# Optimization experiments

Hardware: AMD Instinct MI355X
Metric: run time of the kernel (lower is better)

Reference implementation:

```python
import jax, jax.numpy as jnp
import numpy as np

D_MODEL = 768
NUM_HEADS = 12
D_K = D_MODEL // NUM_HEADS
D_FF = 2048
LN_EPS = 1e-3  # Keras LayerNormalization default
B, S = 4, 2048


def layer_norm(x, gamma, beta):
    mu = jnp.mean(x, axis=-1, keepdims=True)
    var = jnp.var(x, axis=-1, keepdims=True)
    return (x - mu) * jax.lax.rsqrt(var + LN_EPS) * gamma + beta


def setup_inputs() -> dict:
    key = jax.random.key(0)
    ks = jax.random.split(key, 16)
    sd = 0.02
    inp = {
        "x": jax.random.normal(ks[0], (B, S, D_MODEL), dtype=jnp.float32),
        "src_mask": jnp.zeros((B, 1, 1, S), dtype=jnp.float32),
        "Wq": jax.random.normal(ks[1], (D_MODEL, D_MODEL), jnp.float32) * sd,
        "bq": jnp.zeros((D_MODEL,), jnp.float32),
        "Wk": jax.random.normal(ks[2], (D_MODEL, D_MODEL), jnp.float32) * sd,
        "bk": jnp.zeros((D_MODEL,), jnp.float32),
        "Wv": jax.random.normal(ks[3], (D_MODEL, D_MODEL), jnp.float32) * sd,
        "bv": jnp.zeros((D_MODEL,), jnp.float32),
        "Wo": jax.random.normal(ks[4], (D_MODEL, D_MODEL), jnp.float32) * sd,
        "bo": jnp.zeros((D_MODEL,), jnp.float32),
        "W1": jax.random.normal(ks[5], (D_MODEL, D_FF), jnp.float32) * sd,
        "b1": jnp.zeros((D_FF,), jnp.float32),
        "W2": jax.random.normal(ks[6], (D_FF, D_MODEL), jnp.float32) * sd,
        "b2": jnp.zeros((D_MODEL,), jnp.float32),
        "gamma1": jnp.ones((D_MODEL,), jnp.float32),
        "beta1": jnp.zeros((D_MODEL,), jnp.float32),
        "gamma2": jnp.ones((D_MODEL,), jnp.float32),
        "beta2": jnp.zeros((D_MODEL,), jnp.float32),
    }
    return inp


def encoder_layer(x, src_mask, Wq, bq, Wk, bk, Wv, bv, Wo, bo, W1, b1, W2, b2,
                  gamma1, beta1, gamma2, beta2):
    b, s, _ = x.shape
    def heads(t):  # [B,S,D] -> [B,H,S,Dk]
        return t.reshape(b, s, NUM_HEADS, D_K).transpose(0, 2, 1, 3)
    Q = heads(x @ Wq + bq)
    K = heads(x @ Wk + bk)
    V = heads(x @ Wv + bv)
    scores = jnp.einsum("bhqd,bhkd->bhqk", Q, K) / jnp.sqrt(jnp.float32(D_K))
    scores = scores + src_mask * (-1e9)
    probs = jax.nn.softmax(scores, axis=-1)
    attn = jnp.einsum("bhqk,bhkd->bhqd", probs, V)
    attn = attn.transpose(0, 2, 1, 3).reshape(b, s, D_MODEL)
    attn_out = attn @ Wo + bo
    # dropout is identity at inference
    x1 = layer_norm(x + attn_out, gamma1, beta1)
    ff = jax.nn.relu(x1 @ W1 + b1) @ W2 + b2
    return layer_norm(x1 + ff, gamma2, beta2)


def reference(x, src_mask, Wq, bq, Wk, bk, Wv, bv, Wo, bo, W1, b1, W2, b2,
              gamma1, beta1, gamma2, beta2):
    return encoder_layer(x, src_mask, Wq, bq, Wk, bk, Wv, bv, Wo, bo,
                         W1, b1, W2, b2, gamma1, beta1, gamma2, beta2)
```

## Files before the change

kernel.cpp:

```cpp
#include <hip/hip_runtime.h>


typedef unsigned short u16;
typedef __bf16 bf16x8 __attribute__((ext_vector_type(8)));
typedef __bf16 bf16x4 __attribute__((ext_vector_type(4)));
typedef unsigned short u16x8 __attribute__((ext_vector_type(8)));
typedef float f32x4 __attribute__((ext_vector_type(4)));

#define D_MODEL 768
#define D_FF    2048
#define NH      12
#define DK      64
#define S_LEN   2048
#define M_TOK   8192

#define QSCALE   0.18033688011112042f
#define MSCALE  -1.4426950408889634e9f

__device__ __forceinline__ float bf2f(u16 v) {
    union { unsigned u; float f; } c; c.u = ((unsigned)v) << 16; return c.f;
}
__device__ __forceinline__ void st_bf(u16* p, float v) { *(__bf16*)p = (__bf16)v; }

__device__ __forceinline__ void gload_lds16(const void* g, void* l) {
    __builtin_amdgcn_global_load_lds(
        (const __attribute__((address_space(1))) void*)g,
        (__attribute__((address_space(3))) void*)l, 16, 0, 0);
}

__global__ __launch_bounds__(256)
void prep_k(const float* __restrict__ x, const float* __restrict__ Wq,
            const float* __restrict__ Wk, const float* __restrict__ Wv,
            const float* __restrict__ Wo, const float* __restrict__ W1,
            const float* __restrict__ W2, u16* __restrict__ xb,
            u16* __restrict__ WqkvT, u16* __restrict__ WoT,
            u16* __restrict__ W1T, u16* __restrict__ W2T) {
    __shared__ float t[32][33];
    const int id = blockIdx.x, tid = threadIdx.x;
    if (id >= 5376) {
        const int i = ((id - 5376) * 256 + tid) * 4;
        const float4 v = *(const float4*)(x + i);
        __bf16 o[4] = {(__bf16)v.x, (__bf16)v.y, (__bf16)v.z, (__bf16)v.w};
        *(bf16x4*)(xb + i) = *(bf16x4*)o;
        return;
    }
    const float* in; u16* out; int R, C, bx, by;
    if (id < 2304) {
        const int z = id / 576, r = id % 576;
        in = z == 0 ? Wq : (z == 1 ? Wk : (z == 2 ? Wv : Wo));
        out = z == 3 ? WoT : WqkvT + z * 768 * 768;
        R = 768; C = 768; bx = (r % 24) * 32; by = (r / 24) * 32;
    } else if (id < 3840) {
        const int r = id - 2304;
        in = W1; out = W1T; R = 768; C = 2048;
        bx = (r % 64) * 32; by = (r / 64) * 32;
    } else {
        const int r = id - 3840;
        in = W2; out = W2T; R = 2048; C = 768;
        bx = (r % 24) * 32; by = (r / 24) * 32;
    }
    const int tx = tid & 31, ty = tid >> 5;
#pragma unroll
    for (int i = 0; i < 32; i += 8)
        t[ty + i][tx] = in[(size_t)(by + ty + i) * C + bx + tx];
    __syncthreads();
#pragma unroll
    for (int i = 0; i < 32; i += 8)
        st_bf(&out[(size_t)(bx + ty + i) * R + by + tx], t[tx][ty + i]);
}

__global__ __launch_bounds__(256, 2)
void qkv4p_k(const u16* __restrict__ A, const u16* __restrict__ Bt,
             const float* __restrict__ bq, const float* __restrict__ bk,
             const float* __restrict__ bv, u16* __restrict__ Qb,
             u16* __restrict__ Kb, u16* __restrict__ Vt) {
    __shared__ __align__(16) u16 AB[2][16384];
    const int tid = threadIdx.x, lane = tid & 63;
    const int w = tid >> 6;
    const int wm2 = w >> 1, wn2 = w & 1;
    const int r16 = lane & 15, qd = lane >> 4;
    const int qdx = (qd ^ ((r16 >> 1) & 3)) << 3;
    const int m0 = blockIdx.x * 128, n0 = blockIdx.y * 128;
    const int K = D_MODEL, NT = 12;

    const u16* aS[4]; const u16* bS[4];
#pragma unroll
    for (int l = 0; l < 4; ++l) {
        const int f = l * 256 + tid;
        const int row = (f >> 2) & 127, ks = f >> 9;
        const int e = (((f & 3) ^ ((f >> 3) & 3)) << 3);
        aS[l] = A  + (size_t)(m0 + row) * K + ks * 32 + e;
        bS[l] = Bt + (size_t)(n0 + row) * K + ks * 32 + e;
    }

#pragma unroll
    for (int l = 0; l < 4; ++l) {
        gload_lds16(aS[l], &AB[0][(l * 256 + tid) * 8]);
        gload_lds16(bS[l], &AB[0][8192 + (l * 256 + tid) * 8]);
    }
    asm volatile("s_waitcnt vmcnt(0)" ::: "memory");
    __builtin_amdgcn_s_barrier();

    f32x4 acc[4][4] = {};
    bf16x8 af[4][2], bfr[4][2];
    const int arow0 = wm2 * 64 + r16;
    const int brow0 = wn2 * 64 + r16;

    for (int t = 0; t < NT; ++t) {
        const int cur = t & 1, nxt = cur ^ 1;
        const u16* ab = AB[cur];
        const int ka = (t + 1) * 64;
        const bool more = (t + 1) < NT;

#pragma unroll
        for (int mt = 0; mt < 4; ++mt)
#pragma unroll
            for (int ks = 0; ks < 2; ++ks)
                af[mt][ks] = *(const bf16x8*)&ab[ks * 4096 + (arow0 + mt * 16) * 32 + qdx];
#pragma unroll
        for (int nt = 0; nt < 2; ++nt)
#pragma unroll
            for (int ks = 0; ks < 2; ++ks)
                bfr[nt][ks] = *(const bf16x8*)&ab[8192 + ks * 4096 + (brow0 + nt * 16) * 32 + qdx];
        if (more) {
#pragma unroll
            for (int l = 0; l < 4; ++l)
                gload_lds16(aS[l] + ka, &AB[nxt][(l * 256 + tid) * 8]);
        }
        __builtin_amdgcn_s_setprio(1);
#pragma unroll
        for (int mt = 0; mt < 4; ++mt)
#pragma unroll
            for (int nt = 0; nt < 2; ++nt)
#pragma unroll
                for (int ks = 0; ks < 2; ++ks)
                    acc[mt][nt] = __builtin_amdgcn_mfma_f32_16x16x32_bf16(bfr[nt][ks], af[mt][ks], acc[mt][nt], 0, 0, 0);
        __builtin_amdgcn_s_setprio(0);
        __builtin_amdgcn_s_barrier();

#pragma unroll
        for (int nt = 2; nt < 4; ++nt)
#pragma unroll
            for (int ks = 0; ks < 2; ++ks)
                bfr[nt][ks] = *(const bf16x8*)&ab[8192 + ks * 4096 + (brow0 + nt * 16) * 32 + qdx];
        if (more) {
#pragma unroll
            for (int l = 0; l < 4; ++l)
                gload_lds16(bS[l] + ka, &AB[nxt][8192 + (l * 256 + tid) * 8]);
        }
        __builtin_amdgcn_s_setprio(1);
#pragma unroll
        for (int mt = 0; mt < 4; ++mt)
#pragma unroll
            for (int nt = 2; nt < 4; ++nt)
#pragma unroll
                for (int ks = 0; ks < 2; ++ks)
                    acc[mt][nt] = __builtin_amdgcn_mfma_f32_16x16x32_bf16(bfr[nt][ks], af[mt][ks], acc[mt][nt], 0, 0, 0);
        __builtin_amdgcn_s_setprio(0);

        if (more) {
            asm volatile("s_waitcnt vmcnt(0)" ::: "memory");
            __builtin_amdgcn_s_barrier();
        }
    }

    const int sel = n0 < 768 ? 0 : (n0 < 1536 ? 1 : 2);
    const float* bias = sel == 0 ? bq : (sel == 1 ? bk : bv);
    const float scale = sel == 0 ? QSCALE : 1.0f;
    const int nbase = n0 - sel * 768;

#pragma unroll
    for (int nt = 0; nt < 4; ++nt) {
        const int nb = nbase + wn2 * 64 + nt * 16 + qd * 4;
        const float4 bvv = *(const float4*)&bias[nb];
        const float b4[4] = {bvv.x, bvv.y, bvv.z, bvv.w};
#pragma unroll
        for (int mi = 0; mi < 4; ++mi) {
            const int m = m0 + wm2 * 64 + mi * 16 + r16;
            if (sel < 2) {
                __bf16 pk[4];
#pragma unroll
                for (int rr = 0; rr < 4; ++rr)
                    pk[rr] = (__bf16)((acc[mi][nt][rr] + b4[rr]) * scale);
                u16* dst = (sel == 0 ? Qb : Kb) + (size_t)m * D_MODEL + nb;
                *(bf16x4*)dst = *(bf16x4*)pk;
            } else {
                const int bb = m >> 11, npb = m & 2047;
#pragma unroll
                for (int rr = 0; rr < 4; ++rr) {
                    const int col = nb + rr, h = col >> 6, d = col & 63;
                    st_bf(&Vt[(((size_t)(bb * NH + h)) * DK + d) * S_LEN + npb],
                          acc[mi][nt][rr] + b4[rr]);
                }
            }
        }
    }
}

__global__ __launch_bounds__(256, 2)
void g4p_k(const u16* __restrict__ A, const u16* __restrict__ Bt,
           const float* __restrict__ bias, u16* __restrict__ Cout,
           int N, int K) {
    __shared__ __align__(16) u16 AB[2][16384];
    const int tid = threadIdx.x, lane = tid & 63;
    const int w = tid >> 6;
    const int wm2 = w >> 1, wn2 = w & 1;
    const int r16 = lane & 15, qd = lane >> 4;
    const int qdx = (qd ^ ((r16 >> 1) & 3)) << 3;
    const int m0 = blockIdx.x * 128, n0 = blockIdx.y * 128;
    const int NT = K >> 6;

    const u16* aS[4]; const u16* bS[4];
#pragma unroll
    for (int l = 0; l < 4; ++l) {
        const int f = l * 256 + tid;
        const int row = (f >> 2) & 127, ks = f >> 9;
        const int e = (((f & 3) ^ ((f >> 3) & 3)) << 3);
        aS[l] = A  + (size_t)(m0 + row) * K + ks * 32 + e;
        bS[l] = Bt + (size_t)(n0 + row) * K + ks * 32 + e;
    }

#pragma unroll
    for (int l = 0; l < 4; ++l) {
        gload_lds16(aS[l], &AB[0][(l * 256 + tid) * 8]);
        gload_lds16(bS[l], &AB[0][8192 + (l * 256 + tid) * 8]);
    }
    asm volatile("s_waitcnt vmcnt(0)" ::: "memory");
    __builtin_amdgcn_s_barrier();

    f32x4 acc[4][4] = {};
    bf16x8 af[4][2], bfr[4][2];
    const int arow0 = wm2 * 64 + r16;
    const int brow0 = wn2 * 64 + r16;

    for (int t = 0; t < NT; ++t) {
        const int cur = t & 1, nxt = cur ^ 1;
        const u16* ab = AB[cur];
        const int ka = (t + 1) * 64;
        const bool more = (t + 1) < NT;

#pragma unroll
        for (int mt = 0; mt < 4; ++mt)
#pragma unroll
            for (int ks = 0; ks < 2; ++ks)
                af[mt][ks] = *(const bf16x8*)&ab[ks * 4096 + (arow0 + mt * 16) * 32 + qdx];
#pragma unroll
        for (int nt = 0; nt < 2; ++nt)
#pragma unroll
            for (int ks = 0; ks < 2; ++ks)
                bfr[nt][ks] = *(const bf16x8*)&ab[8192 + ks * 4096 + (brow0 + nt * 16) * 32 + qdx];
        if (more) {
#pragma unroll
            for (int l = 0; l < 4; ++l)
                gload_lds16(aS[l] + ka, &AB[nxt][(l * 256 + tid) * 8]);
        }
        __builtin_amdgcn_s_setprio(1);
#pragma unroll
        for (int mt = 0; mt < 4; ++mt)
#pragma unroll
            for (int nt = 0; nt < 2; ++nt)
#pragma unroll
                for (int ks = 0; ks < 2; ++ks)
                    acc[mt][nt] = __builtin_amdgcn_mfma_f32_16x16x32_bf16(bfr[nt][ks], af[mt][ks], acc[mt][nt], 0, 0, 0);
        __builtin_amdgcn_s_setprio(0);
        __builtin_amdgcn_s_barrier();

#pragma unroll
        for (int nt = 2; nt < 4; ++nt)
#pragma unroll
            for (int ks = 0; ks < 2; ++ks)
                bfr[nt][ks] = *(const bf16x8*)&ab[8192 + ks * 4096 + (brow0 + nt * 16) * 32 + qdx];
        if (more) {
#pragma unroll
            for (int l = 0; l < 4; ++l)
                gload_lds16(bS[l] + ka, &AB[nxt][8192 + (l * 256 + tid) * 8]);
        }
        __builtin_amdgcn_s_setprio(1);
#pragma unroll
        for (int mt = 0; mt < 4; ++mt)
#pragma unroll
            for (int nt = 2; nt < 4; ++nt)
#pragma unroll
                for (int ks = 0; ks < 2; ++ks)
                    acc[mt][nt] = __builtin_amdgcn_mfma_f32_16x16x32_bf16(bfr[nt][ks], af[mt][ks], acc[mt][nt], 0, 0, 0);
        __builtin_amdgcn_s_setprio(0);

        if (more) {
            asm volatile("s_waitcnt vmcnt(0)" ::: "memory");
            __builtin_amdgcn_s_barrier();
        }
    }

#pragma unroll
    for (int nt = 0; nt < 4; ++nt) {
        const int nb = n0 + wn2 * 64 + nt * 16 + qd * 4;
        const float4 bv = *(const float4*)&bias[nb];
        const float b4[4] = {bv.x, bv.y, bv.z, bv.w};
#pragma unroll
        for (int mi = 0; mi < 4; ++mi) {
            const int m = m0 + wm2 * 64 + mi * 16 + r16;
            __bf16 pk[4];
#pragma unroll
            for (int rr = 0; rr < 4; ++rr)
                pk[rr] = (__bf16)(acc[mi][nt][rr] + b4[rr]);
            *(bf16x4*)&Cout[(size_t)m * N + nb] = *(bf16x4*)pk;
        }
    }
}

__global__ __launch_bounds__(512, 2)
void ff1_k(const u16* __restrict__ A, const u16* __restrict__ Bt,
           const float* __restrict__ bias, u16* __restrict__ C) {
    __shared__ __align__(16) u16 AB[2][32768];
    const int tid = threadIdx.x, lane = tid & 63;
    const int w = tid >> 6;
    const int wm2 = w >> 2, wn4 = w & 3;
    const int r16 = lane & 15, qd = lane >> 4;
    const int qdx = (qd ^ ((r16 >> 1) & 3)) << 3;
    const int m0 = blockIdx.x * 256, n0 = blockIdx.y * 256;
    const int K = D_MODEL, NT = 12;

    const u16* aS[4]; const u16* bS[4];
#pragma unroll
    for (int l = 0; l < 4; ++l) {
        const int f = l * 512 + tid;
        const int row = (f >> 2) & 255, ks = f >> 10;
        const int e = (((f & 3) ^ ((f >> 3) & 3)) << 3);
        aS[l] = A  + (size_t)(m0 + row) * K + ks * 32 + e;
        bS[l] = Bt + (size_t)(n0 + row) * K + ks * 32 + e;
    }

#pragma unroll
    for (int l = 0; l < 4; ++l) {
        gload_lds16(aS[l], &AB[0][(l * 512 + tid) * 8]);
        gload_lds16(bS[l], &AB[0][16384 + (l * 512 + tid) * 8]);
    }
    asm volatile("s_waitcnt vmcnt(0)" ::: "memory");
    __builtin_amdgcn_s_barrier();

    f32x4 acc[8][4] = {};
    bf16x8 af[4][2], bfr[4][2];
    const int arow0 = wm2 * 128 + r16;
    const int brow0 = wn4 * 64 + r16;

    for (int t = 0; t < NT; ++t) {
        const int cur = t & 1, nxt = cur ^ 1;
        const u16* ab = AB[cur];
        const int ka = (t + 1) * 64;
        const bool more = (t + 1) < NT;

#pragma unroll
        for (int mt = 0; mt < 4; ++mt)
#pragma unroll
            for (int ks = 0; ks < 2; ++ks)
                af[mt][ks] = *(const bf16x8*)&ab[ks * 8192 + (arow0 + mt * 16) * 32 + qdx];
#pragma unroll
        for (int nt = 0; nt < 2; ++nt)
#pragma unroll
            for (int ks = 0; ks < 2; ++ks)
                bfr[nt][ks] = *(const bf16x8*)&ab[16384 + ks * 8192 + (brow0 + nt * 16) * 32 + qdx];
        if (more) {
#pragma unroll
            for (int l = 0; l < 4; ++l)
                gload_lds16(aS[l] + ka, &AB[nxt][(l * 512 + tid) * 8]);
        }
        __builtin_amdgcn_s_setprio(1);
#pragma unroll
        for (int mt = 0; mt < 4; ++mt)
#pragma unroll
            for (int nt = 0; nt < 2; ++nt)
#pragma unroll
                for (int ks = 0; ks < 2; ++ks)
                    acc[mt][nt] = __builtin_amdgcn_mfma_f32_16x16x32_bf16(bfr[nt][ks], af[mt][ks], acc[mt][nt], 0, 0, 0);
        __builtin_amdgcn_s_setprio(0);
        __builtin_amdgcn_s_barrier();

#pragma unroll
        for (int nt = 2; nt < 4; ++nt)
#pragma unroll
            for (int ks = 0; ks < 2; ++ks)
                bfr[nt][ks] = *(const bf16x8*)&ab[16384 + ks * 8192 + (brow0 + nt * 16) * 32 + qdx];
        if (more) {
#pragma unroll
            for (int l = 0; l < 4; ++l)
                gload_lds16(bS[l] + ka, &AB[nxt][16384 + (l * 512 + tid) * 8]);
        }
        __builtin_amdgcn_s_setprio(1);
#pragma unroll
        for (int mt = 0; mt < 4; ++mt)
#pragma unroll
            for (int nt = 2; nt < 4; ++nt)
#pragma unroll
                for (int ks = 0; ks < 2; ++ks)
                    acc[mt][nt] = __builtin_amdgcn_mfma_f32_16x16x32_bf16(bfr[nt][ks], af[mt][ks], acc[mt][nt], 0, 0, 0);
        __builtin_amdgcn_s_setprio(0);
        __builtin_amdgcn_s_barrier();

#pragma unroll
        for (int mt = 0; mt < 4; ++mt)
#pragma unroll
            for (int ks = 0; ks < 2; ++ks)
                af[mt][ks] = *(const bf16x8*)&ab[ks * 8192 + (arow0 + 64 + mt * 16) * 32 + qdx];
        __builtin_amdgcn_s_setprio(1);
#pragma unroll
        for (int mt = 0; mt < 4; ++mt)
#pragma unroll
            for (int nt = 0; nt < 2; ++nt)
#pragma unroll
                for (int ks = 0; ks < 2; ++ks)
                    acc[4 + mt][nt] = __builtin_amdgcn_mfma_f32_16x16x32_bf16(bfr[nt][ks], af[mt][ks], acc[4 + mt][nt], 0, 0, 0);
        __builtin_amdgcn_s_setprio(0);
        __builtin_amdgcn_s_barrier();

        __builtin_amdgcn_s_setprio(1);
#pragma unroll
        for (int mt = 0; mt < 4; ++mt)
#pragma unroll
            for (int nt = 2; nt < 4; ++nt)
#pragma unroll
                for (int ks = 0; ks < 2; ++ks)
                    acc[4 + mt][nt] = __builtin_amdgcn_mfma_f32_16x16x32_bf16(bfr[nt][ks], af[mt][ks], acc[4 + mt][nt], 0, 0, 0);
        __builtin_amdgcn_s_setprio(0);

        if (more) {
            asm volatile("s_waitcnt vmcnt(0)" ::: "memory");
            __builtin_amdgcn_s_barrier();
        }
    }

#pragma unroll
    for (int nt = 0; nt < 4; ++nt) {
        const int nb = n0 + wn4 * 64 + nt * 16 + qd * 4;
        const float4 bv = *(const float4*)&bias[nb];
        const float b4[4] = {bv.x, bv.y, bv.z, bv.w};
#pragma unroll
        for (int mi = 0; mi < 8; ++mi) {
            const int m = m0 + wm2 * 128 + (mi >> 2) * 64 + (mi & 3) * 16 + r16;
            __bf16 pk[4];
#pragma unroll
            for (int rr = 0; rr < 4; ++rr)
                pk[rr] = (__bf16)fmaxf(acc[mi][nt][rr] + b4[rr], 0.0f);
            *(bf16x4*)&C[(size_t)m * D_FF + nb] = *(bf16x4*)pk;
        }
    }
}

#define TS 72

__global__ __launch_bounds__(256, 3)
void attn_k(const u16* __restrict__ Qg, const u16* __restrict__ Kg,
            const u16* __restrict__ Vtg, const float* __restrict__ maskg,
            u16* __restrict__ Og) {
    const int tid = threadIdx.x, lane = tid & 63, w = tid >> 6;
    const int qh = w & 1, kh = w >> 1;
    const int r16 = lane & 15, qd = lane >> 4;
    const int q0 = blockIdx.x * 128;
    const int h = blockIdx.y, b = blockIdx.z;

    __shared__ __align__(16) u16 sm[(64 + 64 + 128) * TS];
    u16* Ks  = sm;
    u16* Vts = sm + 64 * TS;
    u16* Ps  = sm + 128 * TS;

    bf16x8 qa[4][2];
#pragma unroll
    for (int mt = 0; mt < 4; ++mt)
#pragma unroll
        for (int ks = 0; ks < 2; ++ks)
            qa[mt][ks] = *(const bf16x8*)(Qg +
                ((size_t)((b * S_LEN + q0 + qh * 64 + mt * 16 + r16) * NH + h)) * DK +
                ks * 32 + qd * 8);

    const int srow = tid >> 3, sc = (tid & 7) << 3;
    const u16* vsrc = Vtg + (((size_t)(b * NH + h)) * DK) * S_LEN;
    u16x8 kreg[2], vreg[2];
#pragma unroll
    for (int it = 0; it < 2; ++it) {
        const int row = srow + it * 32;
        kreg[it] = *(const u16x8*)(Kg + ((size_t)((b * S_LEN + row) * NH + h)) * DK + sc);
        vreg[it] = *(const u16x8*)(vsrc + (size_t)row * S_LEN + sc);
    }

    float l_i[4] = {0.0f, 0.0f, 0.0f, 0.0f};
    f32x4 Oacc[4][4] = {};

    for (int kt = 0; kt < S_LEN / 64; ++kt) {
        const int ks0 = kt * 64;

#pragma unroll
        for (int it = 0; it < 2; ++it) {
            const int row = srow + it * 32;
            *(u16x8*)&Ks[row * TS + sc]  = kreg[it];
            *(u16x8*)&Vts[row * TS + sc] = vreg[it];
        }

        float4 mrow[2];
#pragma unroll
        for (int nt = 0; nt < 2; ++nt) {
            const float4 mm = ((const float4*)(maskg + (size_t)b * S_LEN + ks0))[kh * 8 + nt * 4 + qd];
            mrow[nt].x = mm.x * MSCALE; mrow[nt].y = mm.y * MSCALE;
            mrow[nt].z = mm.z * MSCALE; mrow[nt].w = mm.w * MSCALE;
        }
        __syncthreads();

        f32x4 sa[4][2];
#pragma unroll
        for (int mt = 0; mt < 4; ++mt)
#pragma unroll
            for (int nt = 0; nt < 2; ++nt) {
                sa[mt][nt][0] = mrow[nt].x; sa[mt][nt][1] = mrow[nt].y;
                sa[mt][nt][2] = mrow[nt].z; sa[mt][nt][3] = mrow[nt].w;
            }
#pragma unroll
        for (int ks = 0; ks < 2; ++ks) {
            bf16x8 kb[2];
#pragma unroll
            for (int nt = 0; nt < 2; ++nt)
                kb[nt] = *(const bf16x8*)&Ks[(kh * 32 + nt * 16 + r16) * TS + ks * 32 + qd * 8];
            __builtin_amdgcn_s_setprio(1);
#pragma unroll
            for (int mt = 0; mt < 4; ++mt)
#pragma unroll
                for (int nt = 0; nt < 2; ++nt)
                    sa[mt][nt] = __builtin_amdgcn_mfma_f32_16x16x32_bf16(kb[nt], qa[mt][ks], sa[mt][nt], 0, 0, 0);
            __builtin_amdgcn_s_setprio(0);
        }

#pragma unroll
        for (int mt = 0; mt < 4; ++mt) {
            float rsum = 0.0f;
#pragma unroll
            for (int nt = 0; nt < 2; ++nt) {
                sa[mt][nt][0] = __builtin_amdgcn_exp2f(sa[mt][nt][0]);
                sa[mt][nt][1] = __builtin_amdgcn_exp2f(sa[mt][nt][1]);
                sa[mt][nt][2] = __builtin_amdgcn_exp2f(sa[mt][nt][2]);
                sa[mt][nt][3] = __builtin_amdgcn_exp2f(sa[mt][nt][3]);
                rsum += sa[mt][nt][0] + sa[mt][nt][1] + sa[mt][nt][2] + sa[mt][nt][3];
            }
            rsum += __shfl_xor(rsum, 16);
            rsum += __shfl_xor(rsum, 32);
            l_i[mt] += rsum;
        }

#pragma unroll
        for (int mt = 0; mt < 4; ++mt)
#pragma unroll
            for (int nt = 0; nt < 2; ++nt) {
                __bf16 pk[4];
#pragma unroll
                for (int rr = 0; rr < 4; ++rr) pk[rr] = (__bf16)sa[mt][nt][rr];
                *(bf16x4*)&Ps[(qh * 64 + mt * 16 + r16) * TS + kh * 32 + nt * 16 + qd * 4] = *(bf16x4*)pk;
            }

        if (kt + 1 < S_LEN / 64) {
            const int ns0 = ks0 + 64;
#pragma unroll
            for (int it = 0; it < 2; ++it) {
                const int row = srow + it * 32;
                kreg[it] = *(const u16x8*)(Kg + ((size_t)((b * S_LEN + ns0 + row) * NH + h)) * DK + sc);
                vreg[it] = *(const u16x8*)(vsrc + (size_t)row * S_LEN + ns0 + sc);
            }
        }

        {
            bf16x8 pa[4], vb[4];
#pragma unroll
            for (int mt = 0; mt < 4; ++mt)
                pa[mt] = *(const bf16x8*)&Ps[(qh * 64 + mt * 16 + r16) * TS + kh * 32 + qd * 8];
#pragma unroll
            for (int vt = 0; vt < 4; ++vt)
                vb[vt] = *(const bf16x8*)&Vts[(vt * 16 + r16) * TS + kh * 32 + qd * 8];
            __builtin_amdgcn_s_setprio(1);
#pragma unroll
            for (int mt = 0; mt < 4; ++mt)
#pragma unroll
                for (int vt = 0; vt < 4; ++vt)
                    Oacc[mt][vt] = __builtin_amdgcn_mfma_f32_16x16x32_bf16(pa[mt], vb[vt], Oacc[mt][vt], 0, 0, 0);
            __builtin_amdgcn_s_setprio(0);
        }
        __syncthreads();
    }

    __syncthreads();
    float* mb  = (float*)sm;
    float* lsm = mb + 128 * 64;
    if (kh == 0) {
#pragma unroll
        for (int mt = 0; mt < 4; ++mt) {
            if (qd == 0) lsm[(qh * 4 + mt) * 16 + r16] = l_i[mt];
#pragma unroll
            for (int vt = 0; vt < 4; ++vt)
#pragma unroll
                for (int rr = 0; rr < 4; ++rr)
                    mb[(qh * 64 + mt * 16 + qd * 4 + rr) * 64 + vt * 16 + r16] = Oacc[mt][vt][rr];
        }
    }
    __syncthreads();
    if (kh == 1) {
#pragma unroll
        for (int mt = 0; mt < 4; ++mt) {
            const float linv = 1.0f / (l_i[mt] + lsm[(qh * 4 + mt) * 16 + r16]);
#pragma unroll
            for (int rr = 0; rr < 4; ++rr) {
                const float lr = __shfl(linv, qd * 4 + rr);
                const int qrow = q0 + qh * 64 + mt * 16 + qd * 4 + rr;
#pragma unroll
                for (int vt = 0; vt < 4; ++vt) {
                    const float o = Oacc[mt][vt][rr] +
                        mb[(qh * 64 + mt * 16 + qd * 4 + rr) * 64 + vt * 16 + r16];
                    st_bf(&Og[((size_t)((b * S_LEN + qrow) * NH + h)) * DK + vt * 16 + r16],
                          o * lr);
                }
            }
        }
    }
}

__global__ __launch_bounds__(256, 4)
void resln_k(const u16* __restrict__ xb, const u16* __restrict__ yb,
             const float* __restrict__ gamma, const float* __restrict__ beta,
             u16* __restrict__ outb, float* __restrict__ outf) {
    const int row = blockIdx.x, tid = threadIdx.x;
    const int lane = tid & 63, w = tid >> 6;
    __shared__ float redS[4], redS2[4];
    const size_t base = (size_t)row * D_MODEL;
    float h[3], s = 0.0f, s2 = 0.0f;
#pragma unroll
    for (int i = 0; i < 3; ++i) {
        const int c = i * 256 + tid;
        const float v = bf2f(xb[base + c]) + bf2f(yb[base + c]);
        h[i] = v; s += v; s2 += v * v;
    }
#pragma unroll
    for (int off = 32; off >= 1; off >>= 1) { s += __shfl_xor(s, off); s2 += __shfl_xor(s2, off); }
    if (lane == 0) { redS[w] = s; redS2[w] = s2; }
    __syncthreads();
    s  = redS[0] + redS[1] + redS[2] + redS[3];
    s2 = redS2[0] + redS2[1] + redS2[2] + redS2[3];
    const float mu  = s * (1.0f / D_MODEL);
    const float var = s2 * (1.0f / D_MODEL) - mu * mu;
    const float rstd = rsqrtf(var + 1e-3f);
#pragma unroll
    for (int i = 0; i < 3; ++i) {
        const int c = i * 256 + tid;
        const float o = (h[i] - mu) * rstd * gamma[c] + beta[c];
        if (outb) st_bf(&outb[base + c], o);
        if (outf) outf[base + c] = o;
    }
}

extern "C" void kernel_launch(void* const* d_in, const int* in_sizes, int n_in,
                              void* d_out, int out_size, void* d_ws, size_t ws_size,
                              hipStream_t stream) {
    (void)in_sizes; (void)n_in; (void)out_size; (void)ws_size;
    const float* x    = (const float*)d_in[0];
    const float* mask = (const float*)d_in[1];
    const float* Wq = (const float*)d_in[2];  const float* bq  = (const float*)d_in[3];
    const float* Wk = (const float*)d_in[4];  const float* bk  = (const float*)d_in[5];
    const float* Wv = (const float*)d_in[6];  const float* bv  = (const float*)d_in[7];
    const float* Wo = (const float*)d_in[8];  const float* bo  = (const float*)d_in[9];
    const float* W1 = (const float*)d_in[10]; const float* b1  = (const float*)d_in[11];
    const float* W2 = (const float*)d_in[12]; const float* b2  = (const float*)d_in[13];
    const float* g1 = (const float*)d_in[14]; const float* be1 = (const float*)d_in[15];
    const float* g2 = (const float*)d_in[16]; const float* be2 = (const float*)d_in[17];

    char* ws = (char*)d_ws;
    u16* xb     = (u16*)(ws + 0);
    u16* WqkvT  = (u16*)(ws + 12582912);
    u16* WoT    = (u16*)(ws + 16121856);
    u16* W1T    = (u16*)(ws + 17301504);
    u16* W2T    = (u16*)(ws + 20447232);
    u16* Qb     = (u16*)(ws + 23592960);
    u16* Kb     = (u16*)(ws + 36175872);
    u16* Vtg    = (u16*)(ws + 48758784);
    u16* Ab     = (u16*)(ws + 61341696);
    u16* Yb     = (u16*)(ws + 73924608);
    u16* X1b    = (u16*)(ws + 86507520);
    u16* H1b    = (u16*)(ws + 23592960);
    u16* Y2b    = (u16*)(ws + 73924608);

    const dim3 blk(256);

    prep_k<<<dim3(11520), blk, 0, stream>>>(x, Wq, Wk, Wv, Wo, W1, W2,
                                            xb, WqkvT, WoT, W1T, W2T);

    qkv4p_k<<<dim3(64, 18), blk, 0, stream>>>(xb, WqkvT, bq, bk, bv, Qb, Kb, Vtg);

    attn_k<<<dim3(16, NH, 4), blk, 0, stream>>>(Qb, Kb, Vtg, mask, Ab);

    g4p_k<<<dim3(64, 6), blk, 0, stream>>>(Ab, WoT, bo, Yb, D_MODEL, D_MODEL);

    resln_k<<<dim3(M_TOK), blk, 0, stream>>>(xb, Yb, g1, be1, X1b, nullptr);

    ff1_k<<<dim3(32, 8), dim3(512), 0, stream>>>(X1b, W1T, b1, H1b);

    g4p_k<<<dim3(64, 6), blk, 0, stream>>>(H1b, W2T, b2, Y2b, D_MODEL, D_FF);

    resln_k<<<dim3(M_TOK), blk, 0, stream>>>(X1b, Y2b, g2, be2, nullptr, (float*)d_out);
}
```

Before: 346.3 us.

## Enlarge QKV GEMM tiles, swap operands for V output, one-wave-per-row LayerNorm

The QKV projection moves from 128x128 tiles with 256 threads to 256x256 tiles with 512 threads and double-buffered 128KB LDS. For the V panel the operands are swapped so the transposed V layout can be written with vectorized 4-element stores instead of scattered scalar stores. The residual LayerNorm now maps one wavefront per row with vector loads and stores and no shared-memory reduction. Larger tiles raise data reuse but cut the grid to 288 blocks and increase register and LDS pressure, which can reduce occupancy.

Measured after the change: 347.2 us. About the same (+0.3%).

```diff
diff --git a/kernel.cpp b/kernel.cpp
--- a/kernel.cpp
+++ b/kernel.cpp
@@ -5,6 +5,7 @@
 typedef __bf16 bf16x8 __attribute__((ext_vector_type(8)));
 typedef __bf16 bf16x4 __attribute__((ext_vector_type(4)));
 typedef unsigned short u16x8 __attribute__((ext_vector_type(8)));
+typedef unsigned short u16x4 __attribute__((ext_vector_type(4)));
 typedef float f32x4 __attribute__((ext_vector_type(4)));
 
 #define D_MODEL 768
@@ -69,42 +70,49 @@
         st_bf(&out[(size_t)(bx + ty + i) * R + by + tx], t[tx][ty + i]);
 }
 
-__global__ __launch_bounds__(256, 2)
-void qkv4p_k(const u16* __restrict__ A, const u16* __restrict__ Bt,
-             const float* __restrict__ bq, const float* __restrict__ bk,
-             const float* __restrict__ bv, u16* __restrict__ Qb,
-             u16* __restrict__ Kb, u16* __restrict__ Vt) {
-    __shared__ __align__(16) u16 AB[2][16384];
+__global__ __launch_bounds__(512, 2)
+void qkv256_k(const u16* __restrict__ A, const u16* __restrict__ Bt,
+              const float* __restrict__ bq, const float* __restrict__ bk,
+              const float* __restrict__ bv, u16* __restrict__ Qb,
+              u16* __restrict__ Kb, u16* __restrict__ Vt) {
+    __shared__ __align__(16) u16 AB[2][32768];
     const int tid = threadIdx.x, lane = tid & 63;
     const int w = tid >> 6;
-    const int wm2 = w >> 1, wn2 = w & 1;
+    const int wm2 = w >> 2, wn4 = w & 3;
     const int r16 = lane & 15, qd = lane >> 4;
     const int qdx = (qd ^ ((r16 >> 1) & 3)) << 3;
-    const int m0 = blockIdx.x * 128, n0 = blockIdx.y * 128;
+    const int m0 = blockIdx.x * 256;
+    const int y = blockIdx.y;
     const int K = D_MODEL, NT = 12;
+    const bool isV = (y >= 6);
+
+    const u16* Apanel = isV ? (Bt + (size_t)(1536 + (y - 6) * 256) * K)
+                            : (A + (size_t)m0 * K);
+    const u16* Bpanel = isV ? (A + (size_t)m0 * K)
+                            : (Bt + (size_t)(y * 256) * K);
 
     const u16* aS[4]; const u16* bS[4];
 #pragma unroll
     for (int l = 0; l < 4; ++l) {
-        const int f = l * 256 + tid;
-        const int row = (f >> 2) & 127, ks = f >> 9;
+        const int f = l * 512 + tid;
+        const int row = (f >> 2) & 255, ks = f >> 10;
         const int e = (((f & 3) ^ ((f >> 3) & 3)) << 3);
-        aS[l] = A  + (size_t)(m0 + row) * K + ks * 32 + e;
-        bS[l] = Bt + (size_t)(n0 + row) * K + ks * 32 + e;
+        aS[l] = Apanel + (size_t)row * K + ks * 32 + e;
+        bS[l] = Bpanel + (size_t)row * K + ks * 32 + e;
     }
 
 #pragma unroll
     for (int l = 0; l < 4; ++l) {
-        gload_lds16(aS[l], &AB[0][(l * 256 + tid) * 8]);
-        gload_lds16(bS[l], &AB[0][8192 + (l * 256 + tid) * 8]);
+        gload_lds16(aS[l], &AB[0][(l * 512 + tid) * 8]);
+        gload_lds16(bS[l], &AB[0][16384 + (l * 512 + tid) * 8]);
     }
     asm volatile("s_waitcnt vmcnt(0)" ::: "memory");
     __builtin_amdgcn_s_barrier();
 
-    f32x4 acc[4][4] = {};
+    f32x4 acc[8][4] = {};
     bf16x8 af[4][2], bfr[4][2];
-    const int arow0 = wm2 * 64 + r16;
-    const int brow0 = wn2 * 64 + r16;
+    const int arow0 = wm2 * 128 + r16;
+    const int brow0 = wn4 * 64 + r16;
 
     for (int t = 0; t < NT; ++t) {
         const int cur = t & 1, nxt = cur ^ 1;
@@ -116,16 +124,16 @@
         for (int mt = 0; mt < 4; ++mt)
 #pragma unroll
             for (int ks = 0; ks < 2; ++ks)
-                af[mt][ks] = *(const bf16x8*)&ab[ks * 4096 + (arow0 + mt * 16) * 32 + qdx];
+                af[mt][ks] = *(const bf16x8*)&ab[ks * 8192 + (arow0 + mt * 16) * 32 + qdx];
 #pragma unroll
         for (int nt = 0; nt < 2; ++nt)
 #pragma unroll
             for (int ks = 0; ks < 2; ++ks)
-                bfr[nt][ks] = *(const bf16x8*)&ab[8192 + ks * 4096 + (brow0 + nt * 16) * 32 + qdx];
+                bfr[nt][ks] = *(const bf16x8*)&ab[16384 + ks * 8192 + (brow0 + nt * 16) * 32 + qdx];
         if (more) {
 #pragma unroll
             for (int l = 0; l < 4; ++l)
-                gload_lds16(aS[l] + ka, &AB[nxt][(l * 256 + tid) * 8]);
+                gload_lds16(aS[l] + ka, &AB[nxt][(l * 512 + tid) * 8]);
         }
         __builtin_amdgcn_s_setprio(1);
 #pragma unroll
@@ -142,11 +150,11 @@
         for (int nt = 2; nt < 4; ++nt)
 #pragma unroll
             for (int ks = 0; ks < 2; ++ks)
-                bfr[nt][ks] = *(const bf16x8*)&ab[8192 + ks * 4096 + (brow0 + nt * 16) * 32 + qdx];
+                bfr[nt][ks] = *(const bf16x8*)&ab[16384 + ks * 8192 + (brow0 + nt * 16) * 32 + qdx];
         if (more) {
 #pragma unroll
             for (int l = 0; l < 4; ++l)
-                gload_lds16(bS[l] + ka, &AB[nxt][8192 + (l * 256 + tid) * 8]);
+                gload_lds16(bS[l] + ka, &AB[nxt][16384 + (l * 512 + tid) * 8]);
         }
         __builtin_amdgcn_s_setprio(1);
 #pragma unroll
@@ -156,6 +164,33 @@
 #pragma unroll
                 for (int ks = 0; ks < 2; ++ks)
                     acc[mt][nt] = __builtin_amdgcn_mfma_f32_16x16x32_bf16(bfr[nt][ks], af[mt][ks], acc[mt][nt], 0, 0, 0);
+        __builtin_amdgcn_s_setprio(0);
+        __builtin_amdgcn_s_barrier();
+
+#pragma unroll
+        for (int mt = 0; mt < 4; ++mt)
+#pragma unroll
+            for (int ks = 0; ks < 2; ++ks)
+                af[mt][ks] = *(const bf16x8*)&ab[ks * 8192 + (arow0 + 64 + mt * 16) * 32 + qdx];
+        __builtin_amdgcn_s_setprio(1);
+#pragma unroll
+        for (int mt = 0; mt < 4; ++mt)
+#pragma unroll
+            for (int nt = 0; nt < 2; ++nt)
+#pragma unroll
+                for (int ks = 0; ks < 2; ++ks)
+                    acc[4 + mt][nt] = __builtin_amdgcn_mfma_f32_16x16x32_bf16(bfr[nt][ks], af[mt][ks], acc[4 + mt][nt], 0, 0, 0);
+        __builtin_amdgcn_s_setprio(0);
+        __builtin_amdgcn_s_barrier();
+
+        __builtin_amdgcn_s_setprio(1);
+#pragma unroll
+        for (int mt = 0; mt < 4; ++mt)
+#pragma unroll
+            for (int nt = 2; nt < 4; ++nt)
+#pragma unroll
+                for (int ks = 0; ks < 2; ++ks)
+                    acc[4 + mt][nt] = __builtin_amdgcn_mfma_f32_16x16x32_bf16(bfr[nt][ks], af[mt][ks], acc[4 + mt][nt], 0, 0, 0);
         __builtin_amdgcn_s_setprio(0);
 
         if (more) {
@@ -164,34 +199,43 @@
         }
     }
 
-    const int sel = n0 < 768 ? 0 : (n0 < 1536 ? 1 : 2);
-    const float* bias = sel == 0 ? bq : (sel == 1 ? bk : bv);
-    const float scale = sel == 0 ? QSCALE : 1.0f;
-    const int nbase = n0 - sel * 768;
-
-#pragma unroll
-    for (int nt = 0; nt < 4; ++nt) {
-        const int nb = nbase + wn2 * 64 + nt * 16 + qd * 4;
-        const float4 bvv = *(const float4*)&bias[nb];
-        const float b4[4] = {bvv.x, bvv.y, bvv.z, bvv.w};
-#pragma unroll
-        for (int mi = 0; mi < 4; ++mi) {
-            const int m = m0 + wm2 * 64 + mi * 16 + r16;
-            if (sel < 2) {
+    if (!isV) {
+        const int sel = y / 3;
+        const float* bias = sel ? bk : bq;
+        const float scale = sel ? 1.0f : QSCALE;
+        const int nbase = y * 256 - sel * 768;
+        u16* dst = sel ? Kb : Qb;
+#pragma unroll
+        for (int nt = 0; nt < 4; ++nt) {
+            const int nb = nbase + wn4 * 64 + nt * 16 + qd * 4;
+            const float4 bv4 = *(const float4*)&bias[nb];
+            const float b4[4] = {bv4.x, bv4.y, bv4.z, bv4.w};
+#pragma unroll
+            for (int mi = 0; mi < 8; ++mi) {
+                const int m = m0 + wm2 * 128 + (mi >> 2) * 64 + (mi & 3) * 16 + r16;
                 __bf16 pk[4];
 #pragma unroll
                 for (int rr = 0; rr < 4; ++rr)
                     pk[rr] = (__bf16)((acc[mi][nt][rr] + b4[rr]) * scale);
-                u16* dst = (sel == 0 ? Qb : Kb) + (size_t)m * D_MODEL + nb;
-                *(bf16x4*)dst = *(bf16x4*)pk;
-            } else {
-                const int bb = m >> 11, npb = m & 2047;
-#pragma unroll
-                for (int rr = 0; rr < 4; ++rr) {
-                    const int col = nb + rr, h = col >> 6, d = col & 63;
-                    st_bf(&Vt[(((size_t)(bb * NH + h)) * DK + d) * S_LEN + npb],
-                          acc[mi][nt][rr] + b4[rr]);
-                }
+                *(bf16x4*)&dst[(size_t)m * D_MODEL + nb] = *(bf16x4*)pk;
+            }
+        }
+    } else {
+        const int d0 = (y - 6) * 256;
+#pragma unroll
+        for (int nt = 0; nt < 4; ++nt) {
+            const int s = m0 + wn4 * 64 + nt * 16 + qd * 4;
+            const int bb = s >> 11, npb = s & 2047;
+#pragma unroll
+            for (int mi = 0; mi < 8; ++mi) {
+                const int d = d0 + wm2 * 128 + (mi >> 2) * 64 + (mi & 3) * 16 + r16;
+                const int h = d >> 6, dd = d & 63;
+                const float bvv = bv[d];
+                __bf16 pk[4];
+#pragma unroll
+                for (int rr = 0; rr < 4; ++rr)
+                    pk[rr] = (__bf16)(acc[mi][nt][rr] + bvv);
+                *(bf16x4*)&Vt[(((size_t)(bb * NH + h)) * DK + dd) * S_LEN + npb] = *(bf16x4*)pk;
             }
         }
     }
@@ -620,32 +664,51 @@
 void resln_k(const u16* __restrict__ xb, const u16* __restrict__ yb,
              const float* __restrict__ gamma, const float* __restrict__ beta,
              u16* __restrict__ outb, float* __restrict__ outf) {
-    const int row = blockIdx.x, tid = threadIdx.x;
-    const int lane = tid & 63, w = tid >> 6;
-    __shared__ float redS[4], redS2[4];
+    const int lane = threadIdx.x & 63, wv = threadIdx.x >> 6;
+    const int row = blockIdx.x * 4 + wv;
     const size_t base = (size_t)row * D_MODEL;
-    float h[3], s = 0.0f, s2 = 0.0f;
-#pragma unroll
-    for (int i = 0; i < 3; ++i) {
-        const int c = i * 256 + tid;
-        const float v = bf2f(xb[base + c]) + bf2f(yb[base + c]);
-        h[i] = v; s += v; s2 += v * v;
-    }
-#pragma unroll
-    for (int off = 32; off >= 1; off >>= 1) { s += __shfl_xor(s, off); s2 += __shfl_xor(s2, off); }
-    if (lane == 0) { redS[w] = s; redS2[w] = s2; }
-    __syncthreads();
-    s  = redS[0] + redS[1] + redS[2] + redS[3];
-    s2 = redS2[0] + redS2[1] + redS2[2] + redS2[3];
+    float h[12];
+    float s = 0.0f, s2 = 0.0f;
+#pragma unroll
+    for (int j = 0; j < 3; ++j) {
+        const int c = lane * 4 + j * 256;
+        const u16x4 xv = *(const u16x4*)(xb + base + c);
+        const u16x4 yv = *(const u16x4*)(yb + base + c);
+#pragma unroll
+        for (int rr = 0; rr < 4; ++rr) {
+            const float v = bf2f(xv[rr]) + bf2f(yv[rr]);
+            h[j * 4 + rr] = v; s += v; s2 += v * v;
+        }
+    }
+#pragma unroll
+    for (int off = 32; off >= 1; off >>= 1) {
+        s  += __shfl_xor(s, off);
+        s2 += __shfl_xor(s2, off);
+    }
     const float mu  = s * (1.0f / D_MODEL);
     const float var = s2 * (1.0f / D_MODEL) - mu * mu;
     const float rstd = rsqrtf(var + 1e-3f);
 #pragma unroll
-    for (int i = 0; i < 3; ++i) {
-        const int c = i * 256 + tid;
-        const float o = (h[i] - mu) * rstd * gamma[c] + beta[c];
-        if (outb) st_bf(&outb[base + c], o);
-        if (outf) outf[base + c] = o;
+    for (int j = 0; j < 3; ++j) {
+        const int c = lane * 4 + j * 256;
+        const float4 g4 = *(const float4*)(gamma + c);
+        const float4 be4 = *(const float4*)(beta + c);
+        const float gg[4] = {g4.x, g4.y, g4.z, g4.w};
+        const float bb[4] = {be4.x, be4.y, be4.z, be4.w};
+        float o[4];
+#pragma unroll
+        for (int rr = 0; rr < 4; ++rr)
+            o[rr] = (h[j * 4 + rr] - mu) * rstd * gg[rr] + bb[rr];
+        if (outb) {
+            __bf16 pk[4];
+#pragma unroll
+            for (int rr = 0; rr < 4; ++rr) pk[rr] = (__bf16)o[rr];
+            *(bf16x4*)(outb + base + c) = *(bf16x4*)pk;
+        }
+        if (outf) {
+            float4 ov = {o[0], o[1], o[2], o[3]};
+            *(float4*)(outf + base + c) = ov;
+        }
     }
 }
 
@@ -684,17 +747,17 @@
     prep_k<<<dim3(11520), blk, 0, stream>>>(x, Wq, Wk, Wv, Wo, W1, W2,
                                             xb, WqkvT, WoT, W1T, W2T);
 
-    qkv4p_k<<<dim3(64, 18), blk, 0, stream>>>(xb, WqkvT, bq, bk, bv, Qb, Kb, Vtg);
+    qkv256_k<<<dim3(32, 9), dim3(512), 0, stream>>>(xb, WqkvT, bq, bk, bv, Qb, Kb, Vtg);
 
     attn_k<<<dim3(16, NH, 4), blk, 0, stream>>>(Qb, Kb, Vtg, mask, Ab);
 
     g4p_k<<<dim3(64, 6), blk, 0, stream>>>(Ab, WoT, bo, Yb, D_MODEL, D_MODEL);
 
-    resln_k<<<dim3(M_TOK), blk, 0, stream>>>(xb, Yb, g1, be1, X1b, nullptr);
+    resln_k<<<dim3(M_TOK / 4), blk, 0, stream>>>(xb, Yb, g1, be1, X1b, nullptr);
 
     ff1_k<<<dim3(32, 8), dim3(512), 0, stream>>>(X1b, W1T, b1, H1b);
 
     g4p_k<<<dim3(64, 6), blk, 0, stream>>>(H1b, W2T, b2, Y2b, D_MODEL, D_FF);
 
-    resln_k<<<dim3(M_TOK), blk, 0, stream>>>(X1b, Y2b, g2, be2, nullptr, (float*)d_out);
-}
+    resln_k<<<dim3(M_TOK / 4), blk, 0, stream>>>(X1b, Y2b, g2, be2, nullptr, (float*)d_out);
+}
```
